# Optimization experiments

Hardware: AMD Instinct MI355X
Metric: run time of the kernel (lower is better)

Reference implementation:

```python
import jax, jax.numpy as jnp
import numpy as np
from jax.scipy.linalg import expm

IN_FEATURES = 1024
EXPDIM = 4
NBLOCKS = IN_FEATURES // EXPDIM  # 256
NLAYERS = 17  # layersize=16 -> 17 LieLinear layers
BATCH = 16384


def setup_inputs() -> dict:
    key = jax.random.key(0)
    k1, k2 = jax.random.split(key)
    data = jax.random.normal(k1, (BATCH, IN_FEATURES), dtype=jnp.float32)
    # v initialized with std = sqrt(1/in_features), as in reset_parameters
    vs = jax.random.normal(k2, (NLAYERS, NBLOCKS, EXPDIM, EXPDIM), dtype=jnp.float32) * np.sqrt(1.0 / IN_FEATURES)
    bs = jnp.zeros((NLAYERS, IN_FEATURES), dtype=jnp.float32)
    # fixed random permutation per layer (created in LieLinear.__init__)
    rng = np.random.default_rng(0)
    idxs = jnp.asarray(np.stack([rng.permutation(IN_FEATURES) for _ in range(NLAYERS)]), dtype=jnp.int32)
    return {"data": data, "vs": vs, "bs": bs, "idxs": idxs}


def _lie_linear(z, logdet, v, b, idx):
    # z: [B, F]; v: [NB, E, E]; b: [F]; idx: [F]
    E = jax.vmap(expm)(v)                      # [NB, E, E] block matrix exponentials
    zb = z.reshape(z.shape[0], NBLOCKS, EXPDIM)
    zb = jnp.einsum('bne,nef->bnf', zb, E)     # batched tiny matmuls
    z = zb.reshape(z.shape[0], IN_FEATURES) + b
    z = z[:, idx]                              # permutation gather
    logdet = logdet - jnp.trace(v, axis1=-2, axis2=-1).sum()
    return z, logdet


def _bent_identity(z, logdet):
    s = jnp.sqrt(z * z + 1.0)
    logdet = logdet - jnp.log(z / (2.0 * s) + 1.0).sum(-1)
    z = (s - 1.0) * 0.5 + z
    return z, logdet


def reference(data, vs, bs, idxs):
    z = data.reshape(-1, IN_FEATURES)
    logdet = jnp.zeros(z.shape[0], dtype=z.dtype)
    # first LieLinear
    z, logdet = _lie_linear(z, logdet, vs[0], bs[0], idxs[0])

    def body(carry, layer):
        z, logdet = carry
        v, b, idx = layer
        z, logdet = _bent_identity(z, logdet)
        z, logdet = _lie_linear(z, logdet, v, b, idx)
        return (z, logdet), None

    (z, logdet), _ = jax.lax.scan(body, (z, logdet), (vs[1:], bs[1:], idxs[1:]))
    return z, logdet
```

## Files before the change

kernel.cpp:

```cpp
#include <hip/hip_runtime.h>
#include <math.h>

#define IN_F    1024
#define NB      256
#define NL      17
#define BATCH_N 16384
#define RPB     8
#define NTRP    (NL * 4)

typedef float v4f __attribute__((ext_vector_type(4)));

__global__ __launch_bounds__(256) void expm_kernel(const float* __restrict__ vs,
                                                   float* __restrict__ E,
                                                   float* __restrict__ tr_part) {
    const int m = blockIdx.x * 256 + threadIdx.x;
    const float* v = vs + (size_t)m * 16;
    float A[16], X[16], P[16], T[16];
    #pragma unroll
    for (int i = 0; i < 16; ++i) A[i] = v[i];
    const float tr = A[0] + A[5] + A[10] + A[15];

    float n1 = 0.0f;
    #pragma unroll
    for (int j = 0; j < 4; ++j) {
        float c = fabsf(A[j]) + fabsf(A[4 + j]) + fabsf(A[8 + j]) + fabsf(A[12 + j]);
        n1 = fmaxf(n1, c);
    }
    int s = 0;
    while (n1 > 0.25f && s < 30) { n1 *= 0.5f; ++s; }
    const float sc = __int_as_float((127 - s) << 23);
    #pragma unroll
    for (int i = 0; i < 16; ++i) { A[i] *= sc; P[i] = A[i]; X[i] = A[i]; }
    X[0] += 1.0f; X[5] += 1.0f; X[10] += 1.0f; X[15] += 1.0f;

    #pragma unroll 1
    for (int k = 2; k <= 9; ++k) {
        const float invk = 1.0f / (float)k;
        #pragma unroll
        for (int i = 0; i < 4; ++i)
            #pragma unroll
            for (int j = 0; j < 4; ++j)
                T[i * 4 + j] = P[i * 4 + 0] * A[0 + j] + P[i * 4 + 1] * A[4 + j] +
                               P[i * 4 + 2] * A[8 + j] + P[i * 4 + 3] * A[12 + j];
        #pragma unroll
        for (int i = 0; i < 16; ++i) { P[i] = T[i] * invk; X[i] += P[i]; }
    }
    #pragma unroll 1
    for (int q = 0; q < s; ++q) {
        #pragma unroll
        for (int i = 0; i < 4; ++i)
            #pragma unroll
            for (int j = 0; j < 4; ++j)
                T[i * 4 + j] = X[i * 4 + 0] * X[0 + j] + X[i * 4 + 1] * X[4 + j] +
                               X[i * 4 + 2] * X[8 + j] + X[i * 4 + 3] * X[12 + j];
        #pragma unroll
        for (int i = 0; i < 16; ++i) X[i] = T[i];
    }
    float* e = E + (size_t)m * 16;
    #pragma unroll
    for (int i = 0; i < 16; ++i) e[i] = X[i];

    float tf = tr;
    #pragma unroll
    for (int off = 32; off > 0; off >>= 1) tf += __shfl_down(tf, off);
    if ((threadIdx.x & 63) == 0)
        tr_part[blockIdx.x * 4 + (threadIdx.x >> 6)] = tf;
}

__global__ __launch_bounds__(256, 4) void flow_kernel(const float* __restrict__ data,
                                                      const float* __restrict__ E,
                                                      const float* __restrict__ bs,
                                                      const int* __restrict__ idxs,
                                                      const float* __restrict__ tr_part,
                                                      float* __restrict__ out) {
    __shared__ float lds[RPB * IN_F];
    __shared__ float red[RPB][4];
    const int t = threadIdx.x;
    const int row0 = blockIdx.x * RPB;

    v4f z[RPB];
    #pragma unroll
    for (int r = 0; r < RPB; ++r)
        z[r] = *(const v4f*)(data + (size_t)(row0 + r) * IN_F + 4 * t);

    float ld2[RPB];
    #pragma unroll
    for (int r = 0; r < RPB; ++r) ld2[r] = 0.0f;

    #pragma unroll 1
    for (int l = 0; l < NL; ++l) {
        if (l > 0) {
            #pragma unroll
            for (int r = 0; r < RPB; ++r) {
                const v4f zz = z[r];
                const v4f q = zz * zz + 1.0f;
                v4f inv;
                inv.x = rsqrtf(q.x); inv.y = rsqrtf(q.y);
                inv.z = rsqrtf(q.z); inv.w = rsqrtf(q.w);
                const v4f sq = q * inv;
                const v4f rat = (0.5f * zz) * inv + 1.0f;
                z[r] = (0.5f * sq + zz) - 0.5f;
                ld2[r] += __log2f((rat.x * rat.y) * (rat.z * rat.w));
            }
        }

        const float* ep = E + ((size_t)l * NB + t) * 16;
        const v4f e0 = *(const v4f*)(ep + 0);
        const v4f e1 = *(const v4f*)(ep + 4);
        const v4f e2 = *(const v4f*)(ep + 8);
        const v4f e3 = *(const v4f*)(ep + 12);
        const v4f bv = *(const v4f*)(bs + (size_t)l * IN_F + 4 * t);
        const int4 id = *(const int4*)(idxs + (size_t)l * IN_F + 4 * t);

        #pragma unroll
        for (int r = 0; r < RPB; ++r) {
            const v4f zz = z[r];
            v4f y = bv;
            y += zz.x * e0;
            y += zz.y * e1;
            y += zz.z * e2;
            y += zz.w * e3;
            *(v4f*)(&lds[r * IN_F + 4 * t]) = y;
        }
        __syncthreads();

        #pragma unroll
        for (int r = 0; r < RPB; ++r) {
            v4f zn;
            zn.x = lds[r * IN_F + id.x];
            zn.y = lds[r * IN_F + id.y];
            zn.z = lds[r * IN_F + id.z];
            zn.w = lds[r * IN_F + id.w];
            z[r] = zn;
        }
        __syncthreads();
    }

    float* out_z = out;
    float* out_ld = out + (size_t)BATCH_N * IN_F;
    #pragma unroll
    for (int r = 0; r < RPB; ++r)
        *(v4f*)(out_z + (size_t)(row0 + r) * IN_F + 4 * t) = z[r];

    float trs = 0.0f;
    const v4f* tp = (const v4f*)tr_part;
    #pragma unroll
    for (int i = 0; i < NL; ++i) {
        const v4f tv = tp[i];
        trs += (tv.x + tv.y) + (tv.z + tv.w);
    }

    #pragma unroll
    for (int r = 0; r < RPB; ++r) {
        float p = ld2[r];
        #pragma unroll
        for (int off = 32; off > 0; off >>= 1) p += __shfl_down(p, off);
        if ((t & 63) == 0) red[r][t >> 6] = p;
    }
    __syncthreads();
    if (t < RPB) {
        const float ssum = red[t][0] + red[t][1] + red[t][2] + red[t][3];
        out_ld[row0 + t] = -trs - 0.6931471805599453f * ssum;
    }
}

extern "C" void kernel_launch(void* const* d_in, const int* in_sizes, int n_in,
                              void* d_out, int out_size, void* d_ws, size_t ws_size,
                              hipStream_t stream) {
    const float* data = (const float*)d_in[0];
    const float* vs   = (const float*)d_in[1];
    const float* bs   = (const float*)d_in[2];
    const int*   idxs = (const int*)d_in[3];

    float* ws      = (float*)d_ws;
    float* tr_part = ws;
    float* E       = ws + 128;

    expm_kernel<<<NL, 256, 0, stream>>>(vs, E, tr_part);
    flow_kernel<<<BATCH_N / RPB, 256, 0, stream>>>(data, E, bs, idxs, tr_part, (float*)d_out);
}
```

Measured before the change: 233.8 us.

## Transpose rows into feature-major v4f lanes with swizzled double-buffered LDS

Cuts rows per block from 8 to 4 and transposes them in registers so each v4f holds one feature across the 4 rows. The permutation gather then becomes one 16-byte LDS read per index instead of four scalar reads. LDS is double-buffered (alternating bufA/bufB by layer), which removes the second barrier per layer, and an XOR swizzle on the v4f index spreads bank accesses. In exchange there are twice as many blocks, and the data, E, bias and index loads are amortized over fewer rows each.

```diff
diff --git a/kernel.cpp b/kernel.cpp
--- a/kernel.cpp
+++ b/kernel.cpp
@@ -5,10 +5,12 @@
 #define NB      256
 #define NL      17
 #define BATCH_N 16384
-#define RPB     8
+#define RPB     4
 #define NTRP    (NL * 4)
 
 typedef float v4f __attribute__((ext_vector_type(4)));
+
+__device__ __forceinline__ int swz(int u) { return u ^ ((u >> 3) & 7); }
 
 __global__ __launch_bounds__(256) void expm_kernel(const float* __restrict__ vs,
                                                    float* __restrict__ E,
@@ -73,35 +75,64 @@
                                                       const int* __restrict__ idxs,
                                                       const float* __restrict__ tr_part,
                                                       float* __restrict__ out) {
-    __shared__ float lds[RPB * IN_F];
+    __shared__ v4f bufA[IN_F];
+    __shared__ v4f bufB[IN_F];
     __shared__ float red[RPB][4];
     const int t = threadIdx.x;
     const int row0 = blockIdx.x * RPB;
 
-    v4f z[RPB];
-    #pragma unroll
-    for (int r = 0; r < RPB; ++r)
-        z[r] = *(const v4f*)(data + (size_t)(row0 + r) * IN_F + 4 * t);
-
-    float ld2[RPB];
-    #pragma unroll
-    for (int r = 0; r < RPB; ++r) ld2[r] = 0.0f;
+    v4f R0 = *(const v4f*)(data + (size_t)(row0 + 0) * IN_F + 4 * t);
+    v4f R1 = *(const v4f*)(data + (size_t)(row0 + 1) * IN_F + 4 * t);
+    v4f R2 = *(const v4f*)(data + (size_t)(row0 + 2) * IN_F + 4 * t);
+    v4f R3 = *(const v4f*)(data + (size_t)(row0 + 3) * IN_F + 4 * t);
+    v4f F0 = { R0.x, R1.x, R2.x, R3.x };
+    v4f F1 = { R0.y, R1.y, R2.y, R3.y };
+    v4f F2 = { R0.z, R1.z, R2.z, R3.z };
+    v4f F3 = { R0.w, R1.w, R2.w, R3.w };
+
+    v4f ld2 = { 0.0f, 0.0f, 0.0f, 0.0f };
 
     #pragma unroll 1
     for (int l = 0; l < NL; ++l) {
         if (l > 0) {
-            #pragma unroll
-            for (int r = 0; r < RPB; ++r) {
-                const v4f zz = z[r];
-                const v4f q = zz * zz + 1.0f;
-                v4f inv;
-                inv.x = rsqrtf(q.x); inv.y = rsqrtf(q.y);
-                inv.z = rsqrtf(q.z); inv.w = rsqrtf(q.w);
-                const v4f sq = q * inv;
-                const v4f rat = (0.5f * zz) * inv + 1.0f;
-                z[r] = (0.5f * sq + zz) - 0.5f;
-                ld2[r] += __log2f((rat.x * rat.y) * (rat.z * rat.w));
-            }
+            v4f rat0, rat1, rat2, rat3;
+            {
+                v4f q = F0 * F0 + 1.0f;
+                v4f inv; inv.x = rsqrtf(q.x); inv.y = rsqrtf(q.y);
+                         inv.z = rsqrtf(q.z); inv.w = rsqrtf(q.w);
+                v4f sq = q * inv;
+                rat0 = F0 * (0.5f * inv) + 1.0f;
+                F0 = 0.5f * sq + (F0 - 0.5f);
+            }
+            {
+                v4f q = F1 * F1 + 1.0f;
+                v4f inv; inv.x = rsqrtf(q.x); inv.y = rsqrtf(q.y);
+                         inv.z = rsqrtf(q.z); inv.w = rsqrtf(q.w);
+                v4f sq = q * inv;
+                rat1 = F1 * (0.5f * inv) + 1.0f;
+                F1 = 0.5f * sq + (F1 - 0.5f);
+            }
+            {
+                v4f q = F2 * F2 + 1.0f;
+                v4f inv; inv.x = rsqrtf(q.x); inv.y = rsqrtf(q.y);
+                         inv.z = rsqrtf(q.z); inv.w = rsqrtf(q.w);
+                v4f sq = q * inv;
+                rat2 = F2 * (0.5f * inv) + 1.0f;
+                F2 = 0.5f * sq + (F2 - 0.5f);
+            }
+            {
+                v4f q = F3 * F3 + 1.0f;
+                v4f inv; inv.x = rsqrtf(q.x); inv.y = rsqrtf(q.y);
+                         inv.z = rsqrtf(q.z); inv.w = rsqrtf(q.w);
+                v4f sq = q * inv;
+                rat3 = F3 * (0.5f * inv) + 1.0f;
+                F3 = 0.5f * sq + (F3 - 0.5f);
+            }
+            const v4f pp = (rat0 * rat1) * (rat2 * rat3);
+            ld2.x += __log2f(pp.x);
+            ld2.y += __log2f(pp.y);
+            ld2.z += __log2f(pp.z);
+            ld2.w += __log2f(pp.w);
         }
 
         const float* ep = E + ((size_t)l * NB + t) * 16;
@@ -112,35 +143,37 @@
         const v4f bv = *(const v4f*)(bs + (size_t)l * IN_F + 4 * t);
         const int4 id = *(const int4*)(idxs + (size_t)l * IN_F + 4 * t);
 
-        #pragma unroll
-        for (int r = 0; r < RPB; ++r) {
-            const v4f zz = z[r];
-            v4f y = bv;
-            y += zz.x * e0;
-            y += zz.y * e1;
-            y += zz.z * e2;
-            y += zz.w * e3;
-            *(v4f*)(&lds[r * IN_F + 4 * t]) = y;
+        v4f* stage = (l & 1) ? bufB : bufA;
+        {
+            v4f y0 = F0 * e0.x + F1 * e1.x + F2 * e2.x + F3 * e3.x + bv.x;
+            v4f y1 = F0 * e0.y + F1 * e1.y + F2 * e2.y + F3 * e3.y + bv.y;
+            v4f y2 = F0 * e0.z + F1 * e1.z + F2 * e2.z + F3 * e3.z + bv.z;
+            v4f y3 = F0 * e0.w + F1 * e1.w + F2 * e2.w + F3 * e3.w + bv.w;
+            stage[swz(4 * t + 0)] = y0;
+            stage[swz(4 * t + 1)] = y1;
+            stage[swz(4 * t + 2)] = y2;
+            stage[swz(4 * t + 3)] = y3;
         }
         __syncthreads();
 
-        #pragma unroll
-        for (int r = 0; r < RPB; ++r) {
-            v4f zn;
-            zn.x = lds[r * IN_F + id.x];
-            zn.y = lds[r * IN_F + id.y];
-            zn.z = lds[r * IN_F + id.z];
-            zn.w = lds[r * IN_F + id.w];
-            z[r] = zn;
-        }
-        __syncthreads();
+        F0 = stage[swz(id.x)];
+        F1 = stage[swz(id.y)];
+        F2 = stage[swz(id.z)];
+        F3 = stage[swz(id.w)];
     }
 
     float* out_z = out;
     float* out_ld = out + (size_t)BATCH_N * IN_F;
-    #pragma unroll
-    for (int r = 0; r < RPB; ++r)
-        *(v4f*)(out_z + (size_t)(row0 + r) * IN_F + 4 * t) = z[r];
+    {
+        v4f w0 = { F0.x, F1.x, F2.x, F3.x };
+        v4f w1 = { F0.y, F1.y, F2.y, F3.y };
+        v4f w2 = { F0.z, F1.z, F2.z, F3.z };
+        v4f w3 = { F0.w, F1.w, F2.w, F3.w };
+        *(v4f*)(out_z + (size_t)(row0 + 0) * IN_F + 4 * t) = w0;
+        *(v4f*)(out_z + (size_t)(row0 + 1) * IN_F + 4 * t) = w1;
+        *(v4f*)(out_z + (size_t)(row0 + 2) * IN_F + 4 * t) = w2;
+        *(v4f*)(out_z + (size_t)(row0 + 3) * IN_F + 4 * t) = w3;
+    }
 
     float trs = 0.0f;
     const v4f* tp = (const v4f*)tr_part;
@@ -150,12 +183,30 @@
         trs += (tv.x + tv.y) + (tv.z + tv.w);
     }
 
-    #pragma unroll
-    for (int r = 0; r < RPB; ++r) {
-        float p = ld2[r];
-        #pragma unroll
-        for (int off = 32; off > 0; off >>= 1) p += __shfl_down(p, off);
-        if ((t & 63) == 0) red[r][t >> 6] = p;
+    const int wid = t >> 6;
+    {
+        float p = ld2.x;
+        #pragma unroll
+        for (int off = 32; off > 0; off >>= 1) p += __shfl_down(p, off);
+        if ((t & 63) == 0) red[0][wid] = p;
+    }
+    {
+        float p = ld2.y;
+        #pragma unroll
+        for (int off = 32; off > 0; off >>= 1) p += __shfl_down(p, off);
+        if ((t & 63) == 0) red[1][wid] = p;
+    }
+    {
+        float p = ld2.z;
+        #pragma unroll
+        for (int off = 32; off > 0; off >>= 1) p += __shfl_down(p, off);
+        if ((t & 63) == 0) red[2][wid] = p;
+    }
+    {
+        float p = ld2.w;
+        #pragma unroll
+        for (int off = 32; off > 0; off >>= 1) p += __shfl_down(p, off);
+        if ((t & 63) == 0) red[3][wid] = p;
     }
     __syncthreads();
     if (t < RPB) {
```

New measurement: 235.6 us. No clear change (+0.8%).
